# Optimization experiments

Measured on AMD Instinct MI355X. Metric: run time of the kernel, lower is better.

Reference implementation:

```python
import jax, jax.numpy as jnp
import numpy as np

STRIDE = 16
MIN_SIZE = 16.0
NMS_THRESH = 0.7
N_PRE = 6000   # n_test_pre_nms
N_POST = 300   # n_test_post_nms
B, C_IN, FH, FW = 2, 256, 50, 50
A_PER = 9


def make_anchors(fh, fw):
    scales = np.array([8.0, 16.0, 32.0])
    ratios = np.array([0.5, 1.0, 2.0])
    ws, hs = [], []
    for r in ratios:
        for s in scales:
            size = s * STRIDE
            ws.append(size * np.sqrt(1.0 / r))
            hs.append(size * np.sqrt(r))
    wh = np.stack([np.array(ws), np.array(hs)], -1).reshape(1, 1, A_PER, 2)
    cx = (np.arange(fw) + 0.5) * STRIDE
    cy = (np.arange(fh) + 0.5) * STRIDE
    cyg, cxg = np.meshgrid(cy, cx, indexing='ij')
    ctr = np.stack([cxg, cyg], -1).reshape(fh, fw, 1, 2)
    anch = np.concatenate([ctr - wh / 2.0, ctr + wh / 2.0], -1)  # [fh,fw,9,4] xyxy
    return anch.reshape(-1, 4).astype(np.float32)


def conv2d(x, w, b, pad):
    y = jax.lax.conv_general_dilated(x, w, (1, 1), pad,
                                     dimension_numbers=('NCHW', 'OIHW', 'NCHW'))
    return y + b[None, :, None, None]


def decode_boxes(anchors, loc, img_w, img_h):
    # anchors [1,A,4] xyxy, loc [B,A,4] (dx,dy,dw,dh)
    aw = anchors[..., 2] - anchors[..., 0]
    ah = anchors[..., 3] - anchors[..., 1]
    acx = anchors[..., 0] + 0.5 * aw
    acy = anchors[..., 1] + 0.5 * ah
    cx = acx + loc[..., 0] * aw
    cy = acy + loc[..., 1] * ah
    w = aw * jnp.exp(loc[..., 2])
    h = ah * jnp.exp(loc[..., 3])
    x1 = jnp.clip(cx - 0.5 * w, 0.0, img_w)
    y1 = jnp.clip(cy - 0.5 * h, 0.0, img_h)
    x2 = jnp.clip(cx + 0.5 * w, 0.0, img_w)
    y2 = jnp.clip(cy + 0.5 * h, 0.0, img_h)
    return jnp.stack([x1, y1, x2, y2], -1)


def pairwise_iou(b):
    area = (b[:, 2] - b[:, 0]) * (b[:, 3] - b[:, 1])
    ix1 = jnp.maximum(b[:, None, 0], b[None, :, 0])
    iy1 = jnp.maximum(b[:, None, 1], b[None, :, 1])
    ix2 = jnp.minimum(b[:, None, 2], b[None, :, 2])
    iy2 = jnp.minimum(b[:, None, 3], b[None, :, 3])
    inter = jnp.clip(ix2 - ix1, 0.0) * jnp.clip(iy2 - iy1, 0.0)
    return inter / (area[:, None] + area[None, :] - inter)


def nms_select(boxes, scores):
    # boxes [N_PRE,4] already sorted by score descending
    iou = jax.lax.stop_gradient(pairwise_iou(boxes))
    idxs = jnp.arange(N_PRE)
    def body(i, keep):
        sup = (iou[i] > NMS_THRESH) & (idxs > i) & keep[i]
        return keep & ~sup
    keep = jax.lax.fori_loop(0, N_PRE, body, jnp.ones((N_PRE,), bool))
    keep = keep & (scores >= 0.0)          # drop invalid (score forced to -1)
    rank = jnp.cumsum(keep)
    sel = keep & (rank <= N_POST)
    order = jnp.argsort(jnp.where(sel, idxs, N_PRE))  # kept idxs first, score order
    top = order[:N_POST]
    m = jnp.arange(N_POST) < jnp.sum(sel)
    out_b = jnp.where(m[:, None], boxes[top], 0.0)
    out_s = jnp.where(m, scores[top], 0.0)
    return out_b, out_s, m


def proposal_pipeline(boxes, scores):
    # per-image: boxes [A,4], scores [A]
    valid = ((boxes[:, 2] - boxes[:, 0]) >= MIN_SIZE) & \
            ((boxes[:, 3] - boxes[:, 1]) >= MIN_SIZE)
    s = jnp.where(valid, scores, -1.0)
    top_s, top_i = jax.lax.top_k(s, N_PRE)
    return nms_select(boxes[top_i], top_s)


def setup_inputs() -> dict:
    k = jax.random.split(jax.random.key(0), 4)
    x = jax.random.normal(k[0], (B, C_IN, FH, FW), jnp.float32)
    conv1_w = 0.01 * jax.random.normal(k[1], (512, C_IN, 3, 3), jnp.float32)
    conv1_b = jnp.zeros((512,), jnp.float32)
    obj_w = 0.01 * jax.random.normal(k[2], (A_PER * 2, 512, 1, 1), jnp.float32)
    obj_b = jnp.zeros((A_PER * 2,), jnp.float32)
    loc_w = 0.01 * jax.random.normal(k[3], (A_PER * 4, 512, 1, 1), jnp.float32)
    loc_b = jnp.zeros((A_PER * 4,), jnp.float32)
    anchor_boxes = jnp.asarray(make_anchors(FH, FW))[None]  # [1, 22500, 4]
    return {"x": x, "conv1_w": conv1_w, "conv1_b": conv1_b,
            "obj_w": obj_w, "obj_b": obj_b, "loc_w": loc_w, "loc_b": loc_b,
            "anchor_boxes": anchor_boxes, "img_h": 800, "img_w": 800}


def reference(x, conv1_w, conv1_b, obj_w, obj_b, loc_w, loc_b, anchor_boxes, img_h, img_w):
    # RPN
    h = jax.nn.relu(conv2d(x, conv1_w, conv1_b, 'SAME'))
    loc = conv2d(h, loc_w, loc_b, 'VALID').transpose(0, 2, 3, 1).reshape(x.shape[0], -1, 4)
    obj = conv2d(h, obj_w, obj_b, 'VALID').transpose(0, 2, 3, 1).reshape(x.shape[0], -1, 2)
    # PreprocessHead: objectness prob, box decode, filter + sort + NMS
    scores = jax.nn.softmax(obj, axis=-1)[..., 1]                       # [B, A]
    boxes = decode_boxes(anchor_boxes[0][None], loc, float(img_w), float(img_h))  # [B, A, 4]
    out_boxes, out_scores, out_mask = jax.vmap(proposal_pipeline)(boxes, scores)
    return out_boxes, out_scores, out_mask
```

## Files before the change

kernel.cpp:

```cpp
#include <hip/hip_runtime.h>
#include <stdint.h>

#define NPOS 2500
#define NANCH 22500
#define NPRE 6000
#define NW 94
#define XPAD 2704
#define CMAX 32
#define KFAST 2048
#define HPART 2560000

__device__ __forceinline__ void gl_lds4(const float* g, float* l) {
  __builtin_amdgcn_global_load_lds((const __attribute__((address_space(1))) void*)g,
                                   (__attribute__((address_space(3))) void*)l, 4, 0, 0);
}
__device__ __forceinline__ void gl_lds16(const float* g, float* l) {
  __builtin_amdgcn_global_load_lds((const __attribute__((address_space(1))) void*)g,
                                   (__attribute__((address_space(3))) void*)l, 16, 0, 0);
}

__global__ __launch_bounds__(256) void prep(const float* __restrict__ w,
                                            float* __restrict__ wt,
                                            const float* __restrict__ x,
                                            float* __restrict__ xp,
                                            const float* __restrict__ objw,
                                            const float* __restrict__ locw,
                                            float* __restrict__ wt54b) {
  __shared__ float tile[32][33];
  int bid = blockIdx.x;
  int tid = threadIdx.x;
  if (bid < 1152) {
    int k0 = (bid % 72) * 32;
    int o0 = (bid / 72) * 32;
    int tx = tid & 31;
    int ty = tid >> 5;
#pragma unroll
    for (int i = 0; i < 4; ++i) {
      int oc = o0 + ty + i * 8;
      int kp = k0 + tx;
      tile[ty + i * 8][tx] = w[(size_t)oc * 2304 + kp];
    }
    __syncthreads();
#pragma unroll
    for (int i = 0; i < 4; ++i) {
      int kp = k0 + ty + i * 8;
      int ic = kp / 9, tap = kp % 9;
      wt[((size_t)tap * 256 + ic) * 512 + (o0 + tx)] = tile[tx][ty + i * 8];
    }
  } else if (bid < 2504) {
    int t = (bid - 1152) * 256 + tid;
    if (t < 2 * 256 * 676) {
      int c = t / 676;
      int q = t % 676;
      int r0 = q * 4;
      float v[4];
#pragma unroll
      for (int k = 0; k < 4; ++k) {
        int r = r0 + k;
        int yy = r / 52, xx = r % 52;
        v[k] = (yy >= 1 && yy <= 50 && xx >= 1 && xx <= 50)
                   ? x[(size_t)c * NPOS + (yy - 1) * 50 + (xx - 1)]
                   : 0.f;
      }
      ((float4*)xp)[t] = make_float4(v[0], v[1], v[2], v[3]);
    }
  } else {
    int t = (bid - 2504) * 256 + tid;
    if (t < 54 * 512) {
      int oc = t / 512, k = t % 512;
      float v = (oc < 18) ? objw[(size_t)oc * 512 + k] : locw[(size_t)(oc - 18) * 512 + k];
      wt54b[((size_t)(k >> 2) * 64 + oc) * 4 + (k & 3)] = v;
    }
  }
}

template <int NSPLIT>
__global__ __launch_bounds__(256) void conv1_gemm_split(const float* __restrict__ xp,
                                                        const float* __restrict__ wt,
                                                        float* __restrict__ hpart) {
  constexpr int ICC_PER = 8 / NSPLIT;
  __shared__ __align__(16) float As[32][128];
  __shared__ __align__(16) float Bs[32][128];
  int b = blockIdx.z;
  int m0 = blockIdx.x * 128;
  int oc0 = (blockIdx.y & 3) * 128;
  int kh = blockIdx.y >> 2;
  int tid = threadIdx.x;
  int lane = tid & 63;
  int wv = tid >> 6;
  int tm = tid >> 4;
  int tn = tid & 15;
  float acc[8][8] = {};

  int p0r = m0 + lane;
  int p0c = p0r < NPOS ? p0r : (NPOS - 1);
  int p1r = m0 + 64 + lane;
  int p1c = p1r < NPOS ? p1r : (NPOS - 1);
  const float* gA0 = xp + (size_t)b * 256 * XPAD + (p0c / 50) * 52 + (p0c % 50) + 53;
  const float* gA1 = xp + (size_t)b * 256 * XPAD + (p1c / 50) * 52 + (p1c % 50) + 53;
  int brow = lane >> 5, bcol4 = (lane & 31) * 4;

  for (int tap = 0; tap < 9; ++tap) {
    int ky = tap / 3 - 1, kx = tap % 3 - 1;
    int koff = ky * 52 + kx;
#pragma unroll
    for (int ii = 0; ii < ICC_PER; ++ii) {
      int ic0 = (kh * ICC_PER + ii) * 32;
      __syncthreads();
#pragma unroll
      for (int j = 0; j < 8; ++j) {
        int kk = wv * 8 + j;
        gl_lds4(gA0 + (size_t)(ic0 + kk) * XPAD + koff, &As[kk][0]);
        gl_lds4(gA1 + (size_t)(ic0 + kk) * XPAD + koff, &As[kk][64]);
      }
#pragma unroll
      for (int q = 0; q < 4; ++q) {
        int r0 = wv * 8 + q * 2;
        gl_lds16(wt + ((size_t)tap * 256 + ic0 + r0 + brow) * 512 + oc0 + bcol4,
                 &Bs[r0][0]);
      }
      __syncthreads();
#pragma unroll 4
      for (int kk = 0; kk < 32; ++kk) {
        float4 a0 = *(const float4*)&As[kk][tm * 4];
        float4 a1 = *(const float4*)&As[kk][64 + tm * 4];
        float4 b0 = *(const float4*)&Bs[kk][tn * 4];
        float4 b1 = *(const float4*)&Bs[kk][64 + tn * 4];
        float am[8] = {a0.x, a0.y, a0.z, a0.w, a1.x, a1.y, a1.z, a1.w};
        float bn[8] = {b0.x, b0.y, b0.z, b0.w, b1.x, b1.y, b1.z, b1.w};
#pragma unroll
        for (int i = 0; i < 8; ++i)
#pragma unroll
          for (int j = 0; j < 8; ++j) acc[i][j] = fmaf(am[i], bn[j], acc[i][j]);
      }
    }
  }
  float* hp = hpart + (size_t)kh * HPART;
#pragma unroll
  for (int i = 0; i < 8; ++i) {
    int row = m0 + ((i & 4) ? 64 : 0) + tm * 4 + (i & 3);
    if (row < NPOS) {
      float* hrow = &hp[((size_t)b * NPOS + row) * 512 + oc0];
      float4 v0 = make_float4(acc[i][0], acc[i][1], acc[i][2], acc[i][3]);
      float4 v1 = make_float4(acc[i][4], acc[i][5], acc[i][6], acc[i][7]);
      *(float4*)&hrow[tn * 4] = v0;
      *(float4*)&hrow[64 + tn * 4] = v1;
    }
  }
}

__global__ __launch_bounds__(256) void conv1_gemm_mono(const float* __restrict__ xp,
                                                       const float* __restrict__ wt,
                                                       const float* __restrict__ bias,
                                                       float* __restrict__ h) {
  __shared__ __align__(16) float As[32][64];
  __shared__ __align__(16) float Bs[32][64];
  int b = blockIdx.z;
  int m0 = blockIdx.x * 64;
  int oc0 = blockIdx.y * 64;
  int tid = threadIdx.x;
  int lane = tid & 63;
  int wv = tid >> 6;
  int tn = tid & 15, tm = tid >> 4;
  float acc[4][4] = {};

  int p = m0 + lane;
  int pc = p < NPOS ? p : (NPOS - 1);
  int py = pc / 50, px = pc % 50;
  const float* gA0 = xp + (size_t)b * 256 * XPAD + py * 52 + px + 53;
  int brow = lane >> 4, bcol4 = (lane & 15) * 4;

  for (int tap = 0; tap < 9; ++tap) {
    int ky = tap / 3 - 1, kx = tap % 3 - 1;
    int koff = ky * 52 + kx;
    for (int icc = 0; icc < 8; ++icc) {
      int ic0 = icc * 32;
      __syncthreads();
#pragma unroll
      for (int j = 0; j < 8; ++j) {
        int kk = wv * 8 + j;
        gl_lds4(gA0 + (size_t)(ic0 + kk) * XPAD + koff, &As[kk][0]);
      }
#pragma unroll
      for (int q = 0; q < 2; ++q) {
        int r0 = wv * 8 + q * 4;
        gl_lds16(wt + ((size_t)tap * 256 + ic0 + r0 + brow) * 512 + oc0 + bcol4,
                 &Bs[r0][0]);
      }
      __syncthreads();
#pragma unroll
      for (int kk = 0; kk < 32; ++kk) {
        float4 av = *(const float4*)&As[kk][tm * 4];
        float4 bv = *(const float4*)&Bs[kk][tn * 4];
        float am[4] = {av.x, av.y, av.z, av.w};
        float bn[4] = {bv.x, bv.y, bv.z, bv.w};
#pragma unroll
        for (int i = 0; i < 4; ++i)
#pragma unroll
          for (int j = 0; j < 4; ++j) acc[i][j] = fmaf(am[i], bn[j], acc[i][j]);
      }
    }
  }
#pragma unroll
  for (int i = 0; i < 4; ++i) {
    int pp = m0 + tm * 4 + i;
    if (pp < NPOS) {
      float4 v;
      float* vp = (float*)&v;
#pragma unroll
      for (int j = 0; j < 4; ++j) {
        int oc = oc0 + tn * 4 + j;
        vp[j] = fmaxf(acc[i][j] + bias[oc], 0.f);
      }
      *(float4*)&h[((size_t)b * NPOS + pp) * 512 + oc0 + tn * 4] = v;
    }
  }
}

template <int NSPLIT>
__global__ __launch_bounds__(256) void heads_t(const float* __restrict__ h,
                                               const float* __restrict__ convb,
                                               const float* __restrict__ wt54b,
                                               const float* __restrict__ objb,
                                               const float* __restrict__ locb,
                                               const float* __restrict__ anch,
                                               const int* __restrict__ imgh,
                                               const int* __restrict__ imgw,
                                               float* __restrict__ scores,
                                               float4* __restrict__ boxes) {
  __shared__ float hv[16 * 512];
  __shared__ float outs[16][64];
  int blk = blockIdx.x;
  int b = blk / 157;
  int p0 = (blk % 157) * 16;
  int tid = threadIdx.x;
  int lane = tid & 63;
  int wv = tid >> 6;
  const float4* h4 = (const float4*)h;
  size_t base = ((size_t)b * NPOS + p0) * 128;
  float4* hv4 = (float4*)hv;
  const float4* cb4 = (const float4*)convb;
#pragma unroll
  for (int q = 0; q < 8; ++q) {
    int f = tid + 256 * q;
    bool ok = (p0 + (f >> 7)) < NPOS;
    if (NSPLIT == 0) {
      hv4[f] = ok ? h4[base + f] : make_float4(0.f, 0.f, 0.f, 0.f);
    } else {
      if (ok) {
        float4 s = h4[base + f];
#pragma unroll
        for (int k = 1; k < NSPLIT; ++k) {
          float4 sk = h4[(size_t)k * (HPART / 4) + base + f];
          s.x += sk.x; s.y += sk.y; s.z += sk.z; s.w += sk.w;
        }
        float4 bb = cb4[f & 127];
        float4 r;
        r.x = fmaxf(s.x + bb.x, 0.f);
        r.y = fmaxf(s.y + bb.y, 0.f);
        r.z = fmaxf(s.z + bb.z, 0.f);
        r.w = fmaxf(s.w + bb.w, 0.f);
        hv4[f] = r;
      } else {
        hv4[f] = make_float4(0.f, 0.f, 0.f, 0.f);
      }
    }
  }
  __syncthreads();
  if (lane < 54) {
    float bias0 = (lane < 18) ? objb[lane] : locb[lane - 18];
    float a0 = bias0, a1 = bias0, a2 = bias0, a3 = bias0;
    const float4* w4 = (const float4*)wt54b;
    int pb = wv * 512;
#pragma unroll 4
    for (int k = 0; k < 128; ++k) {
      float4 wvv = w4[k * 64 + lane];
      float4 h0 = hv4[pb + k], h1 = hv4[pb + 128 + k];
      float4 h2 = hv4[pb + 256 + k], h3 = hv4[pb + 384 + k];
      a0 = fmaf(wvv.x, h0.x, a0); a0 = fmaf(wvv.y, h0.y, a0);
      a0 = fmaf(wvv.z, h0.z, a0); a0 = fmaf(wvv.w, h0.w, a0);
      a1 = fmaf(wvv.x, h1.x, a1); a1 = fmaf(wvv.y, h1.y, a1);
      a1 = fmaf(wvv.z, h1.z, a1); a1 = fmaf(wvv.w, h1.w, a1);
      a2 = fmaf(wvv.x, h2.x, a2); a2 = fmaf(wvv.y, h2.y, a2);
      a2 = fmaf(wvv.z, h2.z, a2); a2 = fmaf(wvv.w, h2.w, a2);
      a3 = fmaf(wvv.x, h3.x, a3); a3 = fmaf(wvv.y, h3.y, a3);
      a3 = fmaf(wvv.z, h3.z, a3); a3 = fmaf(wvv.w, h3.w, a3);
    }
    outs[4 * wv + 0][lane] = a0; outs[4 * wv + 1][lane] = a1;
    outs[4 * wv + 2][lane] = a2; outs[4 * wv + 3][lane] = a3;
  }
  __syncthreads();
  if (lane < 36) {
    int pi = lane / 9, a = lane % 9;
    int p = p0 + 4 * wv + pi;
    if (p < NPOS) {
      float l0 = outs[4 * wv + pi][2 * a], l1 = outs[4 * wv + pi][2 * a + 1];
      float mx = fmaxf(l0, l1);
      float e0 = expf(l0 - mx);
      float e1 = expf(l1 - mx);
      float s = e1 / (e0 + e1);
      float d0 = outs[4 * wv + pi][18 + 4 * a + 0];
      float d1 = outs[4 * wv + pi][18 + 4 * a + 1];
      float d2 = outs[4 * wv + pi][18 + 4 * a + 2];
      float d3 = outs[4 * wv + pi][18 + 4 * a + 3];
      int ai = p * 9 + a;
      float4 A = ((const float4*)anch)[ai];
      float aw = A.z - A.x, ah = A.w - A.y;
      float acx = A.x + 0.5f * aw, acy = A.y + 0.5f * ah;
      float cx = acx + d0 * aw, cy = acy + d1 * ah;
      float w = aw * expf(d2), hh = ah * expf(d3);
      float W = (float)imgw[0], H = (float)imgh[0];
      float x1 = fminf(fmaxf(cx - 0.5f * w, 0.f), W);
      float y1 = fminf(fmaxf(cy - 0.5f * hh, 0.f), H);
      float x2 = fminf(fmaxf(cx + 0.5f * w, 0.f), W);
      float y2 = fminf(fmaxf(cy + 0.5f * hh, 0.f), H);
      bool valid = (x2 - x1 >= 16.f) && (y2 - y1 >= 16.f);
      scores[(size_t)b * NANCH + ai] = valid ? s : -1.f;
      boxes[(size_t)b * NANCH + ai] = make_float4(x1, y1, x2, y2);
    }
  }
}

__device__ inline unsigned int mono_of(float f) {
  unsigned int u = __float_as_uint(f);
  return (u & 0x80000000u) ? ~u : (u | 0x80000000u);
}

__device__ __forceinline__ unsigned int suffix_strict(unsigned int v,
                                                      unsigned int* partw,
                                                      int tid, int lane, int wv) {
  unsigned int inc = v;
#pragma unroll
  for (int d = 1; d < 64; d <<= 1) {
    unsigned int u = __shfl_down(inc, d, 64);
    if (lane + d < 64) inc += u;
  }
  if (lane == 0) partw[wv] = inc;
  __syncthreads();
  if (tid < 16) {
    unsigned int tot = partw[tid];
    unsigned int inc2 = tot;
#pragma unroll
    for (int d = 1; d < 16; d <<= 1) {
      unsigned int u = __shfl_down(inc2, d, 64);
      if (tid + d < 16) inc2 += u;
    }
    partw[tid] = inc2 - tot;
  }
  __syncthreads();
  return partw[wv] + (inc - v);
}

template <int KSEL, int SLOTK, int TBLSZ, int DBITS, bool GATED>
__global__ __launch_bounds__(1024) void topk_sort_t(const float* __restrict__ scores,
                                                    const float4* __restrict__ boxes,
                                                    float* __restrict__ sscore,
                                                    float4* __restrict__ sbox,
                                                    const unsigned int* __restrict__ state) {
  int b = blockIdx.x;
  if (GATED && state[b * 192 + 189]) return;
  const float* sc = scores + (size_t)b * NANCH;
  __shared__ float scL[NANCH];
  __shared__ unsigned int hist[4096];
  __shared__ unsigned int part[1024];
  __shared__ unsigned short pidA[SLOTK * 64];
  __shared__ unsigned short pidB[SLOTK * 64];
  __shared__ unsigned short table[TBLSZ];
  __shared__ int res[8];
  int tid = threadIdx.x;
  int lane = tid & 63;
  int wv = tid >> 6;

  for (int i = tid; i < NANCH; i += 1024) scL[i] = sc[i];
  for (int i = tid; i < 4096; i += 1024) hist[i] = 0;
  __syncthreads();
  for (int i = tid; i < NANCH; i += 1024) atomicAdd(&hist[mono_of(scL[i]) >> 20], 1u);
  __syncthreads();
  {
    unsigned int h0 = hist[4 * tid], h1 = hist[4 * tid + 1];
    unsigned int h2 = hist[4 * tid + 2], h3 = hist[4 * tid + 3];
    unsigned int c = suffix_strict(h0 + h1 + h2 + h3, part, tid, lane, wv);
    const unsigned int need = KSEL;
    if (c < need && c + h3 >= need) { res[0] = 4 * tid + 3; res[1] = (int)c; }
    c += h3;
    if (c < need && c + h2 >= need) { res[0] = 4 * tid + 2; res[1] = (int)c; }
    c += h2;
    if (c < need && c + h1 >= need) { res[0] = 4 * tid + 1; res[1] = (int)c; }
    c += h1;
    if (c < need && c + h0 >= need) { res[0] = 4 * tid + 0; res[1] = (int)c; }
  }
  __syncthreads();
  int t1 = res[0], a1 = res[1];
  __syncthreads();

  for (int i = tid; i < 4096; i += 1024) hist[i] = 0;
  __syncthreads();
  for (int i = tid; i < NANCH; i += 1024) {
    unsigned int m = mono_of(scL[i]);
    if ((int)(m >> 20) == t1) atomicAdd(&hist[(m >> 8) & 0xFFF], 1u);
  }
  __syncthreads();
  {
    unsigned int h0 = hist[4 * tid], h1 = hist[4 * tid + 1];
    unsigned int h2 = hist[4 * tid + 2], h3 = hist[4 * tid + 3];
    unsigned int c = suffix_strict(h0 + h1 + h2 + h3, part, tid, lane, wv);
    const unsigned int need = (unsigned)(KSEL - a1);
    if (c < need && c + h3 >= need) { res[2] = 4 * tid + 3; res[3] = (int)c; }
    c += h3;
    if (c < need && c + h2 >= need) { res[2] = 4 * tid + 2; res[3] = (int)c; }
    c += h2;
    if (c < need && c + h1 >= need) { res[2] = 4 * tid + 1; res[3] = (int)c; }
    c += h1;
    if (c < need && c + h0 >= need) { res[2] = 4 * tid + 0; res[3] = (int)c; }
  }
  __syncthreads();
  int t2 = res[2], a2 = res[3];
  __syncthreads();

  for (int i = tid; i < 256; i += 1024) hist[i] = 0;
  __syncthreads();
  unsigned int top24 = ((unsigned int)t1 << 12) | (unsigned int)t2;
  for (int i = tid; i < NANCH; i += 1024) {
    unsigned int m = mono_of(scL[i]);
    if ((m >> 8) == top24) atomicAdd(&hist[m & 0xFF], 1u);
  }
  __syncthreads();
  {
    unsigned int hb = (tid < 256) ? hist[tid] : 0;
    unsigned int c = suffix_strict(hb, part, tid, lane, wv);
    if (tid < 256) {
      const unsigned int need = (unsigned)(KSEL - a1 - a2);
      if (c < need && c + hb >= need) {
        res[4] = tid;
        res[6] = (int)(need - c);
        res[7] = (hb == need - c) ? NANCH : -1;
      }
    }
  }
  __syncthreads();
  int t3 = res[4];
  unsigned int T = (top24 << 8) | (unsigned int)t3;
  int ties_needed = res[6];
  int idx_cut = res[7];
  __syncthreads();

  if (idx_cut < 0) {
    for (int i = tid; i < 704; i += 1024) hist[i] = 0;
    __syncthreads();
    for (int i = tid; i < NANCH; i += 1024)
      if (mono_of(scL[i]) == T) atomicAdd(&hist[i >> 5], 1u);
    __syncthreads();
    if (tid == 0) {
      int c = 0, cut = NANCH;
      for (int bin = 0; bin < 704; ++bin) {
        int hc = (int)hist[bin];
        if (c + hc >= ties_needed) {
          int c2 = c;
          for (int idx = bin * 32; idx < bin * 32 + 32; ++idx) {
            if (idx < NANCH && mono_of(scL[idx]) == T) {
              ++c2;
              if (c2 == ties_needed) { cut = idx; break; }
            }
          }
          break;
        }
        c += hc;
      }
      res[7] = cut;
    }
    __syncthreads();
    idx_cut = res[7];
    __syncthreads();
  }

  int base0 = tid * 22;
  unsigned int selm = 0;
  int cnt = 0;
  for (int k = 0; k < 22; ++k) {
    int i = base0 + k;
    if (i < NANCH) {
      unsigned int m = mono_of(scL[i]);
      if (m > T || (m == T && i <= idx_cut)) { selm |= 1u << k; ++cnt; }
    }
  }
  {
    int inc = cnt;
#pragma unroll
    for (int d = 1; d < 64; d <<= 1) {
      int u = __shfl_up(inc, d, 64);
      if (lane >= d) inc += u;
    }
    if (lane == 63) part[wv] = (unsigned int)inc;
    __syncthreads();
    if (tid < 16) {
      int v = (int)part[tid];
      int inc2 = v;
#pragma unroll
      for (int d = 1; d < 16; d <<= 1) {
        int u = __shfl_up(inc2, d, 16);
        if (tid >= d) inc2 += u;
      }
      part[tid] = (unsigned int)(inc2 - v);
    }
    __syncthreads();
    int pos = (int)part[wv] + (inc - cnt);
    for (int k = 0; k < 22; ++k)
      if ((selm >> k) & 1u) pidA[pos++] = (unsigned short)(base0 + k);
  }
  __syncthreads();

  unsigned short* src = pidA;
  unsigned short* dst = pidB;
  constexpr int KITER = (SLOTK + 15) / 16;
  constexpr int VPT = TBLSZ / 1024;
  constexpr int PASSES = (32 + DBITS - 1) / DBITS;
  constexpr unsigned int DMASK = (1u << DBITS) - 1u;
  for (int pass = 0; pass < PASSES; ++pass) {
    int shift = pass * DBITS;
    for (int i = tid; i < TBLSZ; i += 1024) table[i] = 0;
    __syncthreads();
    int dig[KITER], irk[KITER], pidr[KITER];
#pragma unroll
    for (int k = 0; k < KITER; ++k) {
      dig[k] = 0; irk[k] = 0; pidr[k] = 0;
      int s = wv + 16 * k;
      if (s < SLOTK) {
        int e = s * 64 + lane;
        bool act = e < KSEL;
        int pid = act ? (int)src[e] : 0;
        unsigned int key = act ? ~mono_of(scL[pid]) : 0u;
        int d = (int)((key >> shift) & DMASK);
        uint64_t peers = __ballot(act);
#pragma unroll
        for (int bb = 0; bb < DBITS; ++bb) {
          uint64_t bl = __ballot(((d >> bb) & 1) != 0);
          peers &= ((d >> bb) & 1) ? bl : ~bl;
        }
        if (act) {
          dig[k] = d;
          pidr[k] = pid;
          irk[k] = (int)__popcll(peers & ((1ull << lane) - 1ull));
          int leader = __ffsll((long long)peers) - 1;
          if (lane == leader)
            table[d * SLOTK + s] = (unsigned short)__popcll(peers);
        }
      }
    }
    __syncthreads();
    {
      int tb = tid * VPT;
      int v[VPT];
      int lsum = 0;
#pragma unroll
      for (int q = 0; q < VPT; ++q) { v[q] = table[tb + q]; lsum += v[q]; }
      int inc = lsum;
#pragma unroll
      for (int d = 1; d < 64; d <<= 1) {
        int u = __shfl_up(inc, d, 64);
        if (lane >= d) inc += u;
      }
      if (lane == 63) part[wv] = (unsigned int)inc;
      __syncthreads();
      if (tid < 16) {
        int vv = (int)part[tid];
        int inc2 = vv;
#pragma unroll
        for (int d = 1; d < 16; d <<= 1) {
          int u = __shfl_up(inc2, d, 16);
          if (tid >= d) inc2 += u;
        }
        part[tid] = (unsigned int)(inc2 - vv);
      }
      __syncthreads();
      int run = (int)part[wv] + (inc - lsum);
#pragma unroll
      for (int q = 0; q < VPT; ++q) { table[tb + q] = (unsigned short)run; run += v[q]; }
    }
    __syncthreads();
#pragma unroll
    for (int k = 0; k < KITER; ++k) {
      int s = wv + 16 * k;
      if (s < SLOTK) {
        int e = s * 64 + lane;
        if (e < KSEL) {
          int pos = (int)table[dig[k] * SLOTK + s] + irk[k];
          dst[pos] = (unsigned short)pidr[k];
        }
      }
    }
    __syncthreads();
    unsigned short* tmp = src; src = dst; dst = tmp;
  }

  for (int r = tid; r < KSEL; r += 1024) {
    int idx = (int)src[r];
    sscore[(size_t)b * NPRE + r] = scL[idx];
    sbox[(size_t)b * NPRE + r] = boxes[(size_t)b * NANCH + idx];
  }
}

__device__ __forceinline__ void iou_compute(const float4* bi, const float4* bj,
                                            uint64_t* __restrict__ M,
                                            int b, int it, int jt, int tid) {
  int li = tid & 63, wq = tid >> 6;
  int i = it * 64 + li;
  int w = jt * 4 + wq;
  if (i < NPRE && w < NW) {
    float4 A = bi[li];
    float areaA = (A.z - A.x) * (A.w - A.y);
    uint64_t bits = 0;
#pragma unroll 8
    for (int jj = 0; jj < 64; ++jj) {
      int j = w * 64 + jj;
      float4 Bx = bj[wq * 64 + jj];
      float ix1 = fmaxf(A.x, Bx.x), iy1 = fmaxf(A.y, Bx.y);
      float ix2 = fminf(A.z, Bx.z), iy2 = fminf(A.w, Bx.w);
      float inter = fmaxf(ix2 - ix1, 0.f) * fmaxf(iy2 - iy1, 0.f);
      float areaB = (Bx.z - Bx.x) * (Bx.w - Bx.y);
      float iou = inter / (areaA + areaB - inter);
      if ((j > i) && (j < NPRE) && (iou > 0.7f)) bits |= (1ull << jj);
    }
    M[((size_t)b * NPRE + i) * NW + w] = bits;
  }
}

__global__ __launch_bounds__(256) void iou_mat(const float4* __restrict__ sbox,
                                               uint64_t* __restrict__ M) {
  __shared__ float4 bi[64];
  __shared__ float4 bj[256];
  int b = blockIdx.z, it = blockIdx.x, jt = blockIdx.y;
  int tid = threadIdx.x;
  if (tid < 64) {
    int i = it * 64 + tid;
    bi[tid] = (i < NPRE) ? sbox[(size_t)b * NPRE + i] : make_float4(0, 0, 0, 0);
  }
  {
    int j = jt * 256 + tid;
    bj[tid] = (j < NPRE) ? sbox[(size_t)b * NPRE + j] : make_float4(0, 0, 0, 0);
  }
  __syncthreads();
  iou_compute(bi, bj, M, b, it, jt, tid);
}

__global__ __launch_bounds__(256) void iou_rest(const float4* __restrict__ sbox,
                                                uint64_t* __restrict__ M,
                                                const unsigned int* __restrict__ state) {
  if (state[blockIdx.z * 192 + 189]) return;
  int it = blockIdx.x, jt16 = blockIdx.y, b = blockIdx.z;
  int tid = threadIdx.x;
  __shared__ float4 bi[64];
  __shared__ float4 bj[256];
  if (tid < 64) {
    int i = it * 64 + tid;
    bi[tid] = (i < NPRE) ? sbox[(size_t)b * NPRE + i] : make_float4(0, 0, 0, 0);
  }
#pragma unroll
  for (int q = 0; q < 4; ++q) {
    int jt = jt16 * 4 + q;
    bool skip = (it < CMAX && jt < CMAX / 4);
    __syncthreads();
    if (!skip) {
      int j = jt * 256 + tid;
      bj[tid] = (j < NPRE) ? sbox[(size_t)b * NPRE + j] : make_float4(0, 0, 0, 0);
    }
    __syncthreads();
    if (!skip) iou_compute(bi, bj, M, b, it, jt, tid);
  }
}

__device__ inline uint64_t shfl64(uint64_t v, int src) {
  int lo = __shfl((int)(unsigned int)(v & 0xFFFFFFFFull), src, 64);
  int hi = __shfl((int)(unsigned int)(v >> 32), src, 64);
  return ((uint64_t)(unsigned int)hi << 32) | (unsigned int)lo;
}

__device__ __forceinline__ void nms_chunk(const uint64_t* __restrict__ Mb,
                                          const float* __restrict__ sscore,
                                          uint64_t* __restrict__ keep,
                                          int b, int c, int tid, int wlimit,
                                          unsigned int* supLo, unsigned int* supHi,
                                          int* klist, int* knS, int* countS,
                                          uint64_t* keptS) {
  int ibase = c * 64;
  if (tid < 64) {
    int lane = tid;
    if (lane == 0) *knS = 0;
    uint64_t supc = ((uint64_t)supHi[c] << 32) | supLo[c];
    uint64_t validm = (c == NW - 1) ? ((1ull << (NPRE - (NW - 1) * 64)) - 1ull) : ~0ull;
    int pos = ibase + lane;
    uint64_t myrow = (pos < NPRE) ? Mb[(size_t)pos * NW + c] : 0ull;
    bool sval = (pos < NPRE) && (sscore[(size_t)b * NPRE + pos] >= 0.f);
    uint64_t vb = __ballot(sval);
    uint64_t cur = validm & ~supc;
    uint64_t kept = 0;
    while (cur) {
      int i = __ffsll((long long)cur) - 1;
      kept |= (1ull << i);
      cur &= ~(1ull << i);
      uint64_t row = shfl64(myrow, i);
      cur &= ~row;
    }
    if (kept & (1ull << lane)) {
      int pp = atomicAdd(knS, 1);
      klist[pp] = lane;
    }
    if (lane == 0) {
      keep[b * NW + c] = kept;
      if (keptS) keptS[c] = kept;
      *countS += __popcll(kept & vb);
    }
  }
  __syncthreads();
  int kn = *knS;
  for (int t = tid; t < kn * 128; t += 1024) {
    int ii = t >> 7, w = t & 127;
    if (w > c && w < wlimit) {
      uint64_t row = Mb[(size_t)(ibase + klist[ii]) * NW + w];
      unsigned int lo = (unsigned int)row;
      unsigned int hi = (unsigned int)(row >> 32);
      if (lo) atomicOr(&supLo[w], lo);
      if (hi) atomicOr(&supHi[w], hi);
    }
  }
  __syncthreads();
}

__global__ __launch_bounds__(1024) void nms_scan(const uint64_t* __restrict__ M,
                                                 const float* __restrict__ sscore,
                                                 uint64_t* __restrict__ keep,
                                                 unsigned int* __restrict__ state,
                                                 const float4* __restrict__ sbox,
                                                 float* __restrict__ out) {
  __shared__ unsigned int supLo[NW], supHi[NW];
  __shared__ int klist[64];
  __shared__ int knS;
  __shared__ int countS;
  __shared__ uint64_t keptS[NW];
  __shared__ int cnt[128];
  __shared__ uint64_t fw[NW];
  int b = blockIdx.x;
  int tid = threadIdx.x;
  const uint64_t* Mb = M + (size_t)b * NPRE * NW;

  for (int w = tid; w < NW; w += 1024) {
    supLo[w] = 0;
    supHi[w] = 0;
    keptS[w] = 0;
    keep[b * NW + w] = 0;
  }
  if (tid == 0) countS = 0;
  __syncthreads();

  int done = 0;
  for (int c = 0; c < CMAX; ++c) {
    nms_chunk(Mb, sscore, keep, b, c, tid, CMAX, supLo, supHi, klist, &knS, &countS, keptS);
    if (countS >= 300) { done = 1; break; }
  }
  __syncthreads();
  unsigned int* st = state + b * 192;
  for (int w = tid; w < NW; w += 1024) { st[w] = supLo[w]; st[94 + w] = supHi[w]; }
  if (tid == 0) { st[188] = (unsigned int)countS; st[189] = (unsigned int)done; }

  if (done) {
    for (int i = tid; i < 1200; i += 1024) out[b * 1200 + i] = 0.f;
    if (tid < 300) {
      out[2400 + b * 300 + tid] = 0.f;
      out[3000 + b * 300 + tid] = 0.f;
    }
    uint64_t fwv = 0;
    if (tid < NW) {
      uint64_t kw = keptS[tid];
      while (kw) {
        int j = __ffsll((long long)kw) - 1;
        kw &= kw - 1;
        if (sscore[(size_t)b * NPRE + tid * 64 + j] >= 0.f) fwv |= (1ull << j);
      }
      fw[tid] = fwv;
    }
    if (tid < 128) cnt[tid] = (tid < NW) ? __popcll(fwv) : 0;
    __syncthreads();
    for (int off = 1; off < 128; off <<= 1) {
      int v = 0, u = 0;
      if (tid < 128) {
        v = cnt[tid];
        u = (tid >= off) ? cnt[tid - off] : 0;
      }
      __syncthreads();
      if (tid < 128) cnt[tid] = v + u;
      __syncthreads();
    }
    if (tid < NW) {
      int base = cnt[tid] - __popcll(fw[tid]);
      uint64_t ww = fw[tid];
      while (ww) {
        int j = __ffsll((long long)ww) - 1;
        ww &= ww - 1;
        if (base < 300) {
          int p = tid * 64 + j;
          float4 bx = sbox[(size_t)b * NPRE + p];
          float* ob = out + b * 1200 + base * 4;
          ob[0] = bx.x; ob[1] = bx.y; ob[2] = bx.z; ob[3] = bx.w;
          out[2400 + b * 300 + base] = sscore[(size_t)b * NPRE + p];
          out[3000 + b * 300 + base] = 1.0f;
        }
        ++base;
      }
    }
  }
}

__global__ __launch_bounds__(1024) void nms_finish(const uint64_t* __restrict__ M,
                                                   const float* __restrict__ sscore,
                                                   uint64_t* __restrict__ keep,
                                                   const unsigned int* __restrict__ state,
                                                   const float4* __restrict__ sbox,
                                                   float* __restrict__ out) {
  __shared__ unsigned int supLo[NW], supHi[NW];
  __shared__ int klist[64];
  __shared__ int knS;
  __shared__ int countS;
  __shared__ int cnt[128];
  __shared__ uint64_t fw[NW];
  int b = blockIdx.x;
  int tid = threadIdx.x;
  const uint64_t* Mb = M + (size_t)b * NPRE * NW;
  const unsigned int* st = state + b * 192;

  if (st[189]) return;

  for (int w = tid; w < NW; w += 1024) { supLo[w] = st[w]; supHi[w] = st[94 + w]; }
  if (tid == 0) countS = (int)st[188];
  __syncthreads();
  for (int c = 0; c < CMAX; ++c) {
    uint64_t kw = keep[b * NW + c];
    if (!kw) continue;
    int ibase = c * 64;
    const int WREST = NW - CMAX;
    for (int t = tid; t < 64 * WREST; t += 1024) {
      int j = t / WREST;
      int w = CMAX + (t % WREST);
      if ((kw >> j) & 1ull) {
        uint64_t row = Mb[(size_t)(ibase + j) * NW + w];
        unsigned int lo = (unsigned int)row;
        unsigned int hi = (unsigned int)(row >> 32);
        if (lo) atomicOr(&supLo[w], lo);
        if (hi) atomicOr(&supHi[w], hi);
      }
    }
  }
  __syncthreads();
  for (int c = CMAX; c < NW; ++c) {
    nms_chunk(Mb, sscore, keep, b, c, tid, NW, supLo, supHi, klist, &knS, &countS, nullptr);
    if (countS >= 300) break;
  }
  __threadfence();
  __syncthreads();

  for (int i = tid; i < 1200; i += 1024) out[b * 1200 + i] = 0.f;
  if (tid < 300) {
    out[2400 + b * 300 + tid] = 0.f;
    out[3000 + b * 300 + tid] = 0.f;
  }
  uint64_t w = 0;
  if (tid < NW) {
    uint64_t kw = keep[b * NW + tid];
    while (kw) {
      int j = __ffsll((long long)kw) - 1;
      kw &= kw - 1;
      if (sscore[(size_t)b * NPRE + tid * 64 + j] >= 0.f) w |= (1ull << j);
    }
    fw[tid] = w;
  }
  if (tid < 128) cnt[tid] = (tid < NW) ? __popcll(w) : 0;
  __syncthreads();
  for (int off = 1; off < 128; off <<= 1) {
    int v = 0, u = 0;
    if (tid < 128) {
      v = cnt[tid];
      u = (tid >= off) ? cnt[tid - off] : 0;
    }
    __syncthreads();
    if (tid < 128) cnt[tid] = v + u;
    __syncthreads();
  }
  if (tid < NW) {
    int base = cnt[tid] - __popcll(fw[tid]);
    uint64_t ww = fw[tid];
    while (ww) {
      int j = __ffsll((long long)ww) - 1;
      ww &= ww - 1;
      if (base < 300) {
        int p = tid * 64 + j;
        float4 bx = sbox[(size_t)b * NPRE + p];
        float* ob = out + b * 1200 + base * 4;
        ob[0] = bx.x; ob[1] = bx.y; ob[2] = bx.z; ob[3] = bx.w;
        out[2400 + b * 300 + base] = sscore[(size_t)b * NPRE + p];
        out[3000 + b * 300 + base] = 1.0f;
      }
      ++base;
    }
  }
}

extern "C" void kernel_launch(void* const* d_in, const int* in_sizes, int n_in,
                              void* d_out, int out_size, void* d_ws, size_t ws_size,
                              hipStream_t stream) {
  const float* x       = (const float*)d_in[0];
  const float* conv1_w = (const float*)d_in[1];
  const float* conv1_b = (const float*)d_in[2];
  const float* obj_w   = (const float*)d_in[3];
  const float* obj_b   = (const float*)d_in[4];
  const float* loc_w   = (const float*)d_in[5];
  const float* loc_b   = (const float*)d_in[6];
  const float* anch    = (const float*)d_in[7];
  const int*   img_h   = (const int*)d_in[8];
  const int*   img_w   = (const int*)d_in[9];

  char* base = (char*)d_ws;
  const size_t NEED8 = 93319424;
  const size_t NEED4 = 52359424;
  int nsplit = (ws_size >= NEED8) ? 8 : (ws_size >= NEED4) ? 4 : 0;

  float* wt = (float*)(base + 0);
  float* h;
  uint64_t* M;
  float* scores;
  float4* boxes;
  float* sscore;
  float4* sbox;
  uint64_t* keep;
  float* xp;
  unsigned int* state;
  float* wt54b;

  size_t off = 4718592;
  h = (float*)(base + off);
  M = (uint64_t*)(base + off);
  off += (nsplit == 8) ? 81920000 : (nsplit == 4) ? 40960000 : 10240000;
  scores = (float*)(base + off); off += 180000;
  boxes  = (float4*)(base + off); off += 720000;
  sscore = (float*)(base + off); off += 48000;
  sbox   = (float4*)(base + off);
  wt54b  = (float*)sbox;
  off += 192000;
  keep   = (uint64_t*)(base + off); off += 1504;
  xp     = (float*)(base + off); off += 5537792;
  state  = (unsigned int*)(base + off);

  hipLaunchKernelGGL(prep, dim3(2612), dim3(256), 0, stream,
                     conv1_w, wt, x, xp, obj_w, loc_w, wt54b);
  if (nsplit == 8) {
    hipLaunchKernelGGL((conv1_gemm_split<8>), dim3(20, 32, 2), dim3(256), 0, stream,
                       xp, wt, h);
    hipLaunchKernelGGL((heads_t<8>), dim3(314), dim3(256), 0, stream, h, conv1_b, wt54b,
                       obj_b, loc_b, anch, img_h, img_w, scores, boxes);
  } else if (nsplit == 4) {
    hipLaunchKernelGGL((conv1_gemm_split<4>), dim3(20, 16, 2), dim3(256), 0, stream,
                       xp, wt, h);
    hipLaunchKernelGGL((heads_t<4>), dim3(314), dim3(256), 0, stream, h, conv1_b, wt54b,
                       obj_b, loc_b, anch, img_h, img_w, scores, boxes);
  } else {
    hipLaunchKernelGGL(conv1_gemm_mono, dim3(40, 8, 2), dim3(256), 0, stream, xp, wt,
                       conv1_b, h);
    hipLaunchKernelGGL((heads_t<0>), dim3(314), dim3(256), 0, stream, h, conv1_b, wt54b,
                       obj_b, loc_b, anch, img_h, img_w, scores, boxes);
  }
  hipLaunchKernelGGL((topk_sort_t<KFAST, 32, 8192, 8, false>), dim3(2), dim3(1024), 0,
                     stream, scores, boxes, sscore, sbox, state);
  hipLaunchKernelGGL(iou_mat, dim3(CMAX, CMAX / 4, 2), dim3(256), 0, stream, sbox, M);
  hipLaunchKernelGGL(nms_scan, dim3(2), dim3(1024), 0, stream, M, sscore, keep, state,
                     sbox, (float*)d_out);
  hipLaunchKernelGGL((topk_sort_t<NPRE, 94, 6144, 6, true>), dim3(2), dim3(1024), 0,
                     stream, scores, boxes, sscore, sbox, state);
  hipLaunchKernelGGL(iou_rest, dim3(NW, 6, 2), dim3(256), 0, stream, sbox, M, state);
  hipLaunchKernelGGL(nms_finish, dim3(2), dim3(1024), 0, stream, M, sscore, keep, state,
                     sbox, (float*)d_out);
}
```

Before: 353.3 us.

## Fuse fast top-k, IoU and NMS scan into one kernel with lazy IoU

```diff
diff --git a/kernel.cpp b/kernel.cpp
--- a/kernel.cpp
+++ b/kernel.cpp
@@ -351,22 +351,15 @@
   return partw[wv] + (inc - v);
 }
 
-template <int KSEL, int SLOTK, int TBLSZ, int DBITS, bool GATED>
-__global__ __launch_bounds__(1024) void topk_sort_t(const float* __restrict__ scores,
-                                                    const float4* __restrict__ boxes,
-                                                    float* __restrict__ sscore,
-                                                    float4* __restrict__ sbox,
-                                                    const unsigned int* __restrict__ state) {
-  int b = blockIdx.x;
-  if (GATED && state[b * 192 + 189]) return;
+template <int KSEL, int SLOTK, int TBLSZ, int DBITS>
+__device__ void topk_core(float* scL, unsigned int* hist, unsigned int* part,
+                          unsigned short* pidA, unsigned short* pidB,
+                          unsigned short* table, int* res,
+                          const float* __restrict__ scores,
+                          const float4* __restrict__ boxes,
+                          float* __restrict__ sscore, float4* __restrict__ sbox,
+                          int b) {
   const float* sc = scores + (size_t)b * NANCH;
-  __shared__ float scL[NANCH];
-  __shared__ unsigned int hist[4096];
-  __shared__ unsigned int part[1024];
-  __shared__ unsigned short pidA[SLOTK * 64];
-  __shared__ unsigned short pidB[SLOTK * 64];
-  __shared__ unsigned short table[TBLSZ];
-  __shared__ int res[8];
   int tid = threadIdx.x;
   int lane = tid & 63;
   int wv = tid >> 6;
@@ -597,6 +590,183 @@
     sscore[(size_t)b * NPRE + r] = scL[idx];
     sbox[(size_t)b * NPRE + r] = boxes[(size_t)b * NANCH + idx];
   }
+}
+
+__global__ __launch_bounds__(1024) void topk_nms(const float* __restrict__ scores,
+                                                 const float4* __restrict__ boxes,
+                                                 float* __restrict__ sscore,
+                                                 float4* __restrict__ sbox,
+                                                 uint64_t* __restrict__ keep,
+                                                 unsigned int* __restrict__ state,
+                                                 float* __restrict__ out) {
+  __shared__ __align__(16) float scL[NANCH];
+  __shared__ unsigned int hist[4096];
+  __shared__ unsigned int part[1024];
+  __shared__ unsigned short pidA[32 * 64];
+  __shared__ unsigned short pidB[32 * 64];
+  __shared__ unsigned short table[8192];
+  __shared__ int res[8];
+  __shared__ unsigned int supLo[CMAX], supHi[CMAX];
+  __shared__ int klist[64];
+  __shared__ int knS;
+  __shared__ int countS;
+  __shared__ uint64_t keptS[CMAX];
+  __shared__ int cnt[128];
+  __shared__ uint64_t fw[CMAX];
+  int b = blockIdx.x;
+  int tid = threadIdx.x;
+  int lane = tid & 63;
+
+  topk_core<KFAST, 32, 8192, 8>(scL, hist, part, pidA, pidB, table, res,
+                                scores, boxes, sscore, sbox, b);
+  __syncthreads();
+
+  float4* sboxL = (float4*)scL;
+  float* sscoreL = scL + 8192;
+  for (int i = tid; i < KFAST; i += 1024) {
+    sboxL[i] = sbox[(size_t)b * NPRE + i];
+    sscoreL[i] = sscore[(size_t)b * NPRE + i];
+  }
+  for (int w = tid; w < CMAX; w += 1024) { supLo[w] = 0; supHi[w] = 0; keptS[w] = 0; }
+  for (int w = tid; w < NW; w += 1024) keep[b * NW + w] = 0;
+  if (tid == 0) countS = 0;
+  __syncthreads();
+
+  int done = 0;
+  for (int c = 0; c < CMAX; ++c) {
+    if (tid < 64) {
+      if (lane == 0) knS = 0;
+      float4 mybox = sboxL[c * 64 + lane];
+      float areaMy = (mybox.z - mybox.x) * (mybox.w - mybox.y);
+      bool sval = sscoreL[c * 64 + lane] >= 0.f;
+      uint64_t vb = __ballot(sval);
+      uint64_t supc = ((uint64_t)supHi[c] << 32) | supLo[c];
+      uint64_t cur = ~supc;
+      uint64_t kept = 0;
+      while (cur) {
+        int i = __ffsll((long long)cur) - 1;
+        kept |= (1ull << i);
+        cur &= ~(1ull << i);
+        float4 A = sboxL[c * 64 + i];
+        float areaA = (A.z - A.x) * (A.w - A.y);
+        float ix1 = fmaxf(A.x, mybox.x), iy1 = fmaxf(A.y, mybox.y);
+        float ix2 = fminf(A.z, mybox.z), iy2 = fminf(A.w, mybox.w);
+        float inter = fmaxf(ix2 - ix1, 0.f) * fmaxf(iy2 - iy1, 0.f);
+        float iou = inter / (areaA + areaMy - inter);
+        uint64_t row = __ballot((lane > i) && (iou > 0.7f));
+        cur &= ~row;
+      }
+      if (kept & (1ull << lane)) {
+        int pp = atomicAdd(&knS, 1);
+        klist[pp] = lane;
+      }
+      if (lane == 0) {
+        keep[b * NW + c] = kept;
+        keptS[c] = kept;
+        countS += __popcll(kept & vb);
+      }
+    }
+    __syncthreads();
+    int kn = knS;
+    int wcount = CMAX - 1 - c;
+    for (int t = tid; t < kn * wcount; t += 1024) {
+      int ii = t / wcount;
+      int w = c + 1 + (t - ii * wcount);
+      int ig = c * 64 + klist[ii];
+      float4 A = sboxL[ig];
+      float areaA = (A.z - A.x) * (A.w - A.y);
+      uint64_t bits = 0;
+#pragma unroll 8
+      for (int jj = 0; jj < 64; ++jj) {
+        int j = w * 64 + jj;
+        float4 Bx = sboxL[j];
+        float ix1 = fmaxf(A.x, Bx.x), iy1 = fmaxf(A.y, Bx.y);
+        float ix2 = fminf(A.z, Bx.z), iy2 = fminf(A.w, Bx.w);
+        float inter = fmaxf(ix2 - ix1, 0.f) * fmaxf(iy2 - iy1, 0.f);
+        float areaB = (Bx.z - Bx.x) * (Bx.w - Bx.y);
+        float iou = inter / (areaA + areaB - inter);
+        if ((j > ig) && (iou > 0.7f)) bits |= (1ull << jj);
+      }
+      unsigned int lo = (unsigned int)bits;
+      unsigned int hi = (unsigned int)(bits >> 32);
+      if (lo) atomicOr(&supLo[w], lo);
+      if (hi) atomicOr(&supHi[w], hi);
+    }
+    __syncthreads();
+    if (countS >= 300) { done = 1; break; }
+  }
+
+  unsigned int* st = state + b * 192;
+  for (int w = tid; w < NW; w += 1024) {
+    st[w] = (w < CMAX) ? supLo[w] : 0u;
+    st[94 + w] = (w < CMAX) ? supHi[w] : 0u;
+  }
+  if (tid == 0) { st[188] = (unsigned int)countS; st[189] = (unsigned int)done; }
+
+  if (done) {
+    for (int i = tid; i < 1200; i += 1024) out[b * 1200 + i] = 0.f;
+    if (tid < 300) {
+      out[2400 + b * 300 + tid] = 0.f;
+      out[3000 + b * 300 + tid] = 0.f;
+    }
+    uint64_t fwv = 0;
+    if (tid < CMAX) {
+      uint64_t kw = keptS[tid];
+      while (kw) {
+        int j = __ffsll((long long)kw) - 1;
+        kw &= kw - 1;
+        if (sscoreL[tid * 64 + j] >= 0.f) fwv |= (1ull << j);
+      }
+      fw[tid] = fwv;
+    }
+    if (tid < 128) cnt[tid] = (tid < CMAX) ? __popcll(fwv) : 0;
+    __syncthreads();
+    for (int off = 1; off < 128; off <<= 1) {
+      int v = 0, u = 0;
+      if (tid < 128) {
+        v = cnt[tid];
+        u = (tid >= off) ? cnt[tid - off] : 0;
+      }
+      __syncthreads();
+      if (tid < 128) cnt[tid] = v + u;
+      __syncthreads();
+    }
+    if (tid < CMAX) {
+      int base2 = cnt[tid] - __popcll(fw[tid]);
+      uint64_t ww = fw[tid];
+      while (ww) {
+        int j = __ffsll((long long)ww) - 1;
+        ww &= ww - 1;
+        if (base2 < 300) {
+          int p = tid * 64 + j;
+          float4 bx = sboxL[p];
+          float* ob = out + b * 1200 + base2 * 4;
+          ob[0] = bx.x; ob[1] = bx.y; ob[2] = bx.z; ob[3] = bx.w;
+          out[2400 + b * 300 + base2] = sscoreL[p];
+          out[3000 + b * 300 + base2] = 1.0f;
+        }
+        ++base2;
+      }
+    }
+  }
+}
+
+__global__ __launch_bounds__(1024) void topk_full_gated(const float* __restrict__ scores,
+                                                        const float4* __restrict__ boxes,
+                                                        float* __restrict__ sscore,
+                                                        float4* __restrict__ sbox,
+                                                        const unsigned int* __restrict__ state) {
+  int b = blockIdx.x;
+  if (state[b * 192 + 189]) return;
+  __shared__ __align__(16) float scL[NANCH];
+  __shared__ unsigned int hist[4096];
+  __shared__ unsigned int part[1024];
+  __shared__ unsigned short pidA[94 * 64];
+  __shared__ unsigned short pidB[94 * 64];
+  __shared__ unsigned short table[6144];
+  __shared__ int res[8];
+  topk_core<NPRE, 94, 6144, 6>(scL, hist, part, pidA, pidB, table, res,
+                               scores, boxes, sscore, sbox, b);
 }
 
 __device__ __forceinline__ void iou_compute(const float4* bi, const float4* bj,
@@ -624,24 +794,6 @@
   }
 }
 
-__global__ __launch_bounds__(256) void iou_mat(const float4* __restrict__ sbox,
-                                               uint64_t* __restrict__ M) {
-  __shared__ float4 bi[64];
-  __shared__ float4 bj[256];
-  int b = blockIdx.z, it = blockIdx.x, jt = blockIdx.y;
-  int tid = threadIdx.x;
-  if (tid < 64) {
-    int i = it * 64 + tid;
-    bi[tid] = (i < NPRE) ? sbox[(size_t)b * NPRE + i] : make_float4(0, 0, 0, 0);
-  }
-  {
-    int j = jt * 256 + tid;
-    bj[tid] = (j < NPRE) ? sbox[(size_t)b * NPRE + j] : make_float4(0, 0, 0, 0);
-  }
-  __syncthreads();
-  iou_compute(bi, bj, M, b, it, jt, tid);
-}
-
 __global__ __launch_bounds__(256) void iou_rest(const float4* __restrict__ sbox,
                                                 uint64_t* __restrict__ M,
                                                 const unsigned int* __restrict__ state) {
@@ -657,14 +809,13 @@
 #pragma unroll
   for (int q = 0; q < 4; ++q) {
     int jt = jt16 * 4 + q;
-    bool skip = (it < CMAX && jt < CMAX / 4);
-    __syncthreads();
-    if (!skip) {
+    __syncthreads();
+    {
       int j = jt * 256 + tid;
       bj[tid] = (j < NPRE) ? sbox[(size_t)b * NPRE + j] : make_float4(0, 0, 0, 0);
     }
     __syncthreads();
-    if (!skip) iou_compute(bi, bj, M, b, it, jt, tid);
+    iou_compute(bi, bj, M, b, it, jt, tid);
   }
 }
 
@@ -725,90 +876,6 @@
   __syncthreads();
 }
 
-__global__ __launch_bounds__(1024) void nms_scan(const uint64_t* __restrict__ M,
-                                                 const float* __restrict__ sscore,
-                                                 uint64_t* __restrict__ keep,
-                                                 unsigned int* __restrict__ state,
-                                                 const float4* __restrict__ sbox,
-                                                 float* __restrict__ out) {
-  __shared__ unsigned int supLo[NW], supHi[NW];
-  __shared__ int klist[64];
-  __shared__ int knS;
-  __shared__ int countS;
-  __shared__ uint64_t keptS[NW];
-  __shared__ int cnt[128];
-  __shared__ uint64_t fw[NW];
-  int b = blockIdx.x;
-  int tid = threadIdx.x;
-  const uint64_t* Mb = M + (size_t)b * NPRE * NW;
-
-  for (int w = tid; w < NW; w += 1024) {
-    supLo[w] = 0;
-    supHi[w] = 0;
-    keptS[w] = 0;
-    keep[b * NW + w] = 0;
-  }
-  if (tid == 0) countS = 0;
-  __syncthreads();
-
-  int done = 0;
-  for (int c = 0; c < CMAX; ++c) {
-    nms_chunk(Mb, sscore, keep, b, c, tid, CMAX, supLo, supHi, klist, &knS, &countS, keptS);
-    if (countS >= 300) { done = 1; break; }
-  }
-  __syncthreads();
-  unsigned int* st = state + b * 192;
-  for (int w = tid; w < NW; w += 1024) { st[w] = supLo[w]; st[94 + w] = supHi[w]; }
-  if (tid == 0) { st[188] = (unsigned int)countS; st[189] = (unsigned int)done; }
-
-  if (done) {
-    for (int i = tid; i < 1200; i += 1024) out[b * 1200 + i] = 0.f;
-    if (tid < 300) {
-      out[2400 + b * 300 + tid] = 0.f;
-      out[3000 + b * 300 + tid] = 0.f;
-    }
-    uint64_t fwv = 0;
-    if (tid < NW) {
-      uint64_t kw = keptS[tid];
-      while (kw) {
-        int j = __ffsll((long long)kw) - 1;
-        kw &= kw - 1;
-        if (sscore[(size_t)b * NPRE + tid * 64 + j] >= 0.f) fwv |= (1ull << j);
-      }
-      fw[tid] = fwv;
-    }
-    if (tid < 128) cnt[tid] = (tid < NW) ? __popcll(fwv) : 0;
-    __syncthreads();
-    for (int off = 1; off < 128; off <<= 1) {
-      int v = 0, u = 0;
-      if (tid < 128) {
-        v = cnt[tid];
-        u = (tid >= off) ? cnt[tid - off] : 0;
-      }
-      __syncthreads();
-      if (tid < 128) cnt[tid] = v + u;
-      __syncthreads();
-    }
-    if (tid < NW) {
-      int base = cnt[tid] - __popcll(fw[tid]);
-      uint64_t ww = fw[tid];
-      while (ww) {
-        int j = __ffsll((long long)ww) - 1;
-        ww &= ww - 1;
-        if (base < 300) {
-          int p = tid * 64 + j;
-          float4 bx = sbox[(size_t)b * NPRE + p];
-          float* ob = out + b * 1200 + base * 4;
-          ob[0] = bx.x; ob[1] = bx.y; ob[2] = bx.z; ob[3] = bx.w;
-          out[2400 + b * 300 + base] = sscore[(size_t)b * NPRE + p];
-          out[3000 + b * 300 + base] = 1.0f;
-        }
-        ++base;
-      }
-    }
-  }
-}
-
 __global__ __launch_bounds__(1024) void nms_finish(const uint64_t* __restrict__ M,
                                                    const float* __restrict__ sscore,
                                                    uint64_t* __restrict__ keep,
@@ -965,13 +1032,10 @@
     hipLaunchKernelGGL((heads_t<0>), dim3(314), dim3(256), 0, stream, h, conv1_b, wt54b,
                        obj_b, loc_b, anch, img_h, img_w, scores, boxes);
   }
-  hipLaunchKernelGGL((topk_sort_t<KFAST, 32, 8192, 8, false>), dim3(2), dim3(1024), 0,
-                     stream, scores, boxes, sscore, sbox, state);
-  hipLaunchKernelGGL(iou_mat, dim3(CMAX, CMAX / 4, 2), dim3(256), 0, stream, sbox, M);
-  hipLaunchKernelGGL(nms_scan, dim3(2), dim3(1024), 0, stream, M, sscore, keep, state,
-                     sbox, (float*)d_out);
-  hipLaunchKernelGGL((topk_sort_t<NPRE, 94, 6144, 6, true>), dim3(2), dim3(1024), 0,
-                     stream, scores, boxes, sscore, sbox, state);
+  hipLaunchKernelGGL(topk_nms, dim3(2), dim3(1024), 0, stream,
+                     scores, boxes, sscore, sbox, keep, state, (float*)d_out);
+  hipLaunchKernelGGL(topk_full_gated, dim3(2), dim3(1024), 0, stream,
+                     scores, boxes, sscore, sbox, state);
   hipLaunchKernelGGL(iou_rest, dim3(NW, 6, 2), dim3(256), 0, stream, sbox, M, state);
   hipLaunchKernelGGL(nms_finish, dim3(2), dim3(1024), 0, stream, M, sscore, keep, state,
                      sbox, (float*)d_out);
```

Result: slower. 570.2 us (+61.4%).
